# Kernel optimization log

Hardware: AMD Instinct MI355X
Metric: run time of the kernel (lower is better)

Reference implementation:

```python
import jax, jax.numpy as jnp
import numpy as np

EMBEDDING_DIM = 64
NUM_EMBEDDINGS = 512
COMMITMENT_COST = 0.25
DECAY = 0.99
EPSILON = 1e-5


def setup_inputs() -> dict:
    key = jax.random.key(0)
    k1, k2 = jax.random.split(key)
    inputs = jax.random.normal(k1, (64, 32, 32, EMBEDDING_DIM), dtype=jnp.float32)
    # VarianceScaling(uniform) init over [D, K]: scale ~ sqrt(3/fan_in)
    limit = np.sqrt(3.0 / EMBEDDING_DIM)
    embeddings = jax.random.uniform(
        k2, (EMBEDDING_DIM, NUM_EMBEDDINGS), dtype=jnp.float32,
        minval=-limit, maxval=limit)
    return {
        "inputs": inputs,
        "embeddings": embeddings,
        "ema_cluster_size_hidden": jnp.zeros((NUM_EMBEDDINGS,), jnp.float32),
        "ema_dw_hidden": jnp.zeros((EMBEDDING_DIM, NUM_EMBEDDINGS), jnp.float32),
        "counter": 0,  # EMA step counter before this call
    }


def reference(inputs, embeddings, ema_cluster_size_hidden, ema_dw_hidden, counter):
    # is_training=True path of VectorQuantizerEMA.__call__
    flat = inputs.reshape(-1, EMBEDDING_DIM)                        # [N, D]
    # squared L2 distances to each codebook vector: [N, K]
    distances = (jnp.sum(jnp.square(flat), 1, keepdims=True)
                 - 2.0 * jnp.matmul(flat, embeddings)
                 + jnp.sum(jnp.square(embeddings), 0, keepdims=True))
    encoding_indices_flat = jnp.argmax(-distances, 1)               # [N]
    encodings = jax.nn.one_hot(encoding_indices_flat, NUM_EMBEDDINGS,
                               dtype=distances.dtype)               # [N, K]
    encoding_indices = encoding_indices_flat.reshape(inputs.shape[:-1])
    quantized = embeddings.T[encoding_indices]                      # gather rows of [K, D]

    e_latent_loss = jnp.mean(jnp.square(jax.lax.stop_gradient(quantized) - inputs))
    loss = COMMITMENT_COST * e_latent_loss

    # --- EMA updates (haiku ExponentialMovingAverage with zero-debias) ---
    new_counter = counter + 1
    debias = 1.0 - DECAY ** new_counter
    cluster_size = jnp.sum(encodings, axis=0)                        # [K]
    hid_cs = ema_cluster_size_hidden * DECAY + cluster_size * (1.0 - DECAY)
    updated_ema_cluster_size = hid_cs / debias
    dw = jnp.matmul(flat.T, encodings)                               # [D, K]
    hid_dw = ema_dw_hidden * DECAY + dw * (1.0 - DECAY)
    updated_ema_dw = hid_dw / debias

    n = jnp.sum(updated_ema_cluster_size)
    stable_cs = ((updated_ema_cluster_size + EPSILON)
                 / (n + NUM_EMBEDDINGS * EPSILON) * n)
    new_embeddings = updated_ema_dw / stable_cs[None, :]             # [D, K]

    # straight-through estimator
    quantized_st = inputs + jax.lax.stop_gradient(quantized - inputs)

    avg_probs = jnp.mean(encodings, 0)
    perplexity = jnp.exp(-jnp.sum(avg_probs * jnp.log(avg_probs + 1e-10)))

    return (quantized_st, loss, perplexity, encoding_indices,
            new_embeddings, hid_cs, hid_dw)
```

## Files before the change

### kernel.cpp

```cpp
#include <hip/hip_runtime.h>
#include <math.h>

#define D 64
#define K 512
#define NROWS 65536
#define DECAY 0.99f
#define ONE_MINUS_DECAY (1.0f - 0.99f)
#define COMMIT 0.25f

#define WS_DWT    0
#define WS_CNT    32768
#define WS_LPART  33280
#define WS_ZERO4  8192
#define WS_ESQ    35328
#define WS_ET     35840
#define WS_EF     68608
#define WS_IDX    101376
#define WS_HIST   166912
#define WS_PERM   35840

#define OUT_Q     0
#define OUT_LOSS  4194304
#define OUT_PERP  4194305
#define OUT_IDX   4194306
#define OUT_NEMB  4259842
#define OUT_HCS   4292610
#define OUT_HDW   4293122

typedef _Float16 f16x8 __attribute__((ext_vector_type(8)));
typedef float    f32x16 __attribute__((ext_vector_type(16)));

__global__ void vq_prep(const float* __restrict__ emb,
                        float* __restrict__ ws)
{
    int i = blockIdx.x * 256 + threadIdx.x;
    if (i < WS_ZERO4) {
        ((float4*)ws)[i] = make_float4(0.f, 0.f, 0.f, 0.f);
    }
    if (i < K * D) {
        int k = i >> 6, d = i & 63;
        ws[WS_ET + i] = emb[d * K + k];
    }
    if (i < K) {
        float s = 0.f;
        for (int d = 0; d < D; ++d) { float v = emb[d * K + i]; s += v * v; }
        ws[WS_ESQ + i] = s;
    }
    if (i < 8192) {
        int l = i & 63, h = (i >> 6) & 1, s = (i >> 7) & 3, t = i >> 9;
        int col = t * 32 + (l & 31);
        int d0  = s * 16 + ((l >> 5) << 3);
        f16x8 frag;
#pragma unroll
        for (int j = 0; j < 8; ++j) {
            float v = emb[(d0 + j) * K + col];
            _Float16 hv = (_Float16)v;
            frag[j] = h ? (_Float16)(v - (float)hv) : hv;
        }
        ((f16x8*)(ws + WS_EF))[i] = frag;
    }
}

__global__ __launch_bounds__(256, 4)
void vq_main(const float* __restrict__ x,
             const float* __restrict__ e_sq,
             const float* __restrict__ e_t,
             const float* __restrict__ ef,
             float* __restrict__ out_q,
             float* __restrict__ out_idx,
             int*   __restrict__ idxN,
             float* __restrict__ lparts)
{
    __shared__ float sc_s[4][32];
    __shared__ int   id_s[4][32];
    __shared__ int   idx_f[32];

    const int tid  = threadIdx.x;
    const int w    = tid >> 6;
    const int l    = tid & 63;
    const int lr   = l & 31;
    const int hb   = l >> 5;
    const int row0 = blockIdx.x * 32;

    f16x8 ah[4], al[4];
    float xsq = 0.f;
    {
        const float* xr = x + (size_t)(row0 + lr) * D + hb * 8;
#pragma unroll
        for (int s = 0; s < 4; ++s) {
            float4 f0 = *(const float4*)(xr + s * 16);
            float4 f1 = *(const float4*)(xr + s * 16 + 4);
            float f[8] = {f0.x, f0.y, f0.z, f0.w, f1.x, f1.y, f1.z, f1.w};
#pragma unroll
            for (int j = 0; j < 8; ++j) {
                xsq = fmaf(f[j], f[j], xsq);
                _Float16 hv = (_Float16)f[j];
                ah[s][j] = hv;
                al[s][j] = (_Float16)(f[j] - (float)hv);
            }
        }
    }

    float    best[16];
    unsigned pack = 0u;
#pragma unroll
    for (int r = 0; r < 16; ++r) best[r] = 3.0e38f;

    const f16x8* __restrict__ efv = (const f16x8*)ef;

#pragma unroll 2
    for (int tt = 0; tt < 4; ++tt) {
        const int t = w * 4 + tt;
        f32x16 acc = {};
#pragma unroll
        for (int s = 0; s < 4; ++s) {
            f16x8 bh = efv[(t * 8 + s * 2 + 0) * 64 + l];
            f16x8 bl = efv[(t * 8 + s * 2 + 1) * 64 + l];
            acc = __builtin_amdgcn_mfma_f32_32x32x16_f16(al[s], bh, acc, 0, 0, 0);
            acc = __builtin_amdgcn_mfma_f32_32x32x16_f16(ah[s], bl, acc, 0, 0, 0);
            acc = __builtin_amdgcn_mfma_f32_32x32x16_f16(ah[s], bh, acc, 0, 0, 0);
        }

        const float eq = e_sq[t * 32 + lr];
#pragma unroll
        for (int r = 0; r < 16; ++r) {
            float sc = fmaf(-2.0f, acc[r], eq);
            bool better = sc < best[r];
            unsigned nb = (pack & ~(3u << (2 * r)))
                        | ((unsigned)tt << (2 * r));
            best[r] = better ? sc : best[r];
            pack    = better ? nb : pack;
        }
    }

#pragma unroll
    for (int r = 0; r < 16; ++r) {
        float b  = best[r];
        int   bk = (w * 4 + (int)((pack >> (2 * r)) & 3u)) * 32 + lr;
#pragma unroll
        for (int m = 16; m >= 1; m >>= 1) {
            float ob  = __shfl_xor(b, m, 64);
            int   obk = __shfl_xor(bk, m, 64);
            if (ob < b || (ob == b && obk < bk)) { b = ob; bk = obk; }
        }
        if (lr == 0) {
            int row = (r & 3) + 8 * (r >> 2) + 4 * hb;
            sc_s[w][row] = b;
            id_s[w][row] = bk;
        }
    }

    float xs_total = 0.f;
    if (w == 0) {
        float xs = xsq;
#pragma unroll
        for (int m = 32; m >= 1; m >>= 1) xs += __shfl_xor(xs, m, 64);
        xs_total = xs;
    }
    __syncthreads();

    if (tid < 32) {
        float b = sc_s[0][tid]; int bk = id_s[0][tid];
#pragma unroll
        for (int w2 = 1; w2 < 4; ++w2) {
            float ob = sc_s[w2][tid];
            int  obk = id_s[w2][tid];
            if (ob < b) { b = ob; bk = obk; }
        }
        idx_f[tid] = bk;
        out_idx[row0 + tid] = (float)bk;
        idxN[row0 + tid]    = bk;

        float lb = b;
#pragma unroll
        for (int m = 16; m >= 1; m >>= 1) lb += __shfl_xor(lb, m, 64);
        if (tid == 0)
            lparts[blockIdx.x] = lb + xs_total;
    }
    __syncthreads();

#pragma unroll
    for (int rr = 0; rr < 8; ++rr) {
        const int row = w * 8 + rr;
        const int kk  = idx_f[row];
        out_q[(size_t)(row0 + row) * D + l] = e_t[kk * D + l];
    }
}

__global__ __launch_bounds__(256)
void vq_hist(const int* __restrict__ idxN,
             int* __restrict__ hist)
{
    __shared__ int h[K];
    const int t = threadIdx.x;
    h[t] = 0; h[t + 256] = 0;
    __syncthreads();
    const int base = blockIdx.x * 1024;
#pragma unroll
    for (int it = 0; it < 4; ++it)
        atomicAdd(&h[idxN[base + it * 256 + t]], 1);
    __syncthreads();
    hist[blockIdx.x * K + t]       = h[t];
    hist[blockIdx.x * K + t + 256] = h[t + 256];
}

__global__ __launch_bounds__(512)
void vq_scatter(const int* __restrict__ hist,
                const int* __restrict__ idxN,
                int* __restrict__ cnt,
                int* __restrict__ perm)
{
    __shared__ int s[K];

    const int t = threadIdx.x;
    const int b = blockIdx.x;

    int run = 0, mybase = 0;
    for (int b2 = 0; b2 < 64; ++b2) {
        int h = hist[b2 * K + t];
        if (b2 == b) mybase = run;
        run += h;
    }
    if (b == 0) cnt[t] = run;

    s[t] = run;
    __syncthreads();
#pragma unroll
    for (int off = 1; off < K; off <<= 1) {
        int v = (t >= off) ? s[t - off] : 0;
        __syncthreads();
        s[t] += v;
        __syncthreads();
    }
    const int offs = s[t] - run;
    __syncthreads();
    s[t] = offs + mybase;
    __syncthreads();

#pragma unroll
    for (int it = 0; it < 2; ++it) {
        int row = b * 1024 + it * 512 + t;
        int kk  = idxN[row];
        int pos = atomicAdd(&s[kk], 1);
        perm[pos] = (row << 9) | kk;
    }
}

__global__ __launch_bounds__(256, 2)
void vq_dwsum(const int* __restrict__ perm,
              const float* __restrict__ x,
              float* __restrict__ dw_t)
{
    const int w = (blockIdx.x * 256 + threadIdx.x) >> 6;
    const int l = threadIdx.x & 63;

    int pv = 0;
    if (l < 32) pv = perm[w * 32 + l];

    float sum = 0.f;
    int kcur = -1;
#pragma unroll
    for (int e = 0; e < 32; ++e) {
        int pe  = __shfl(pv, e, 64);
        int kk  = pe & (K - 1);
        int row = pe >> 9;
        float xv = x[(size_t)row * D + l];
        if (kk != kcur) {
            if (kcur >= 0) atomicAdd(&dw_t[kcur * D + l], sum);
            kcur = kk; sum = xv;
        } else {
            sum += xv;
        }
    }
    atomicAdd(&dw_t[kcur * D + l], sum);
}

__global__ __launch_bounds__(256)
void vq_final(const int*   __restrict__ cnt,
              const float* __restrict__ lparts,
              const float* __restrict__ ema_csh,
              const int*   __restrict__ counter,
              const float* __restrict__ ema_dwh,
              const float* __restrict__ dw_t,
              float* __restrict__ out_loss,
              float* __restrict__ out_perp,
              float* __restrict__ out_hcs,
              float* __restrict__ out_nemb,
              float* __restrict__ out_hdw)
{
    __shared__ float s_red[4], s_red2[4];
    __shared__ float s_n;

    const int tid = threadIdx.x;
    const int b   = blockIdx.x;

    const int   cntr   = counter[0] + 1;
    const float debias = 1.0f - powf(DECAY, (float)cntr);

    const float c0 = (float)cnt[tid];
    const float c1 = (float)cnt[tid + 256];
    const float hid0 = ema_csh[tid] * DECAY + c0 * ONE_MINUS_DECAY;
    const float hid1 = ema_csh[tid + 256] * DECAY + c1 * ONE_MINUS_DECAY;
    const float upd0 = hid0 / debias;
    const float upd1 = hid1 / debias;

    float v = upd0 + upd1;
#pragma unroll
    for (int m = 32; m >= 1; m >>= 1) v += __shfl_xor(v, m, 64);
    if ((tid & 63) == 0) s_red[tid >> 6] = v;
    __syncthreads();
    if (tid == 0) s_n = s_red[0] + s_red[1] + s_red[2] + s_red[3];
    __syncthreads();
    const float n = s_n;

    const int i  = b * 256 + tid;
    const int kk = i & (K - 1);
    const int d  = i >> 9;
    const float updk   = (b & 1) ? upd1 : upd0;
    const float stable = (updk + 1e-5f) / (n + (float)K * 1e-5f) * n;
    const float hdw = ema_dwh[i] * DECAY + dw_t[kk * D + d] * ONE_MINUS_DECAY;
    out_hdw[i]  = hdw;
    out_nemb[i] = (hdw / debias) / stable;

    if (b == 0) {
        out_hcs[tid]       = hid0;
        out_hcs[tid + 256] = hid1;

        const float inv = 1.0f / (float)NROWS;
        float p0 = c0 * inv, p1 = c1 * inv;
        float ve = p0 * logf(p0 + 1e-10f) + p1 * logf(p1 + 1e-10f);
        float lp = 0.f;
#pragma unroll
        for (int j = 0; j < 8; ++j) lp += lparts[tid + 256 * j];
#pragma unroll
        for (int m = 32; m >= 1; m >>= 1) {
            ve += __shfl_xor(ve, m, 64);
            lp += __shfl_xor(lp, m, 64);
        }
        __syncthreads();
        if ((tid & 63) == 0) { s_red[tid >> 6] = ve; s_red2[tid >> 6] = lp; }
        __syncthreads();
        if (tid == 0) {
            float e = s_red[0] + s_red[1] + s_red[2] + s_red[3];
            float L = s_red2[0] + s_red2[1] + s_red2[2] + s_red2[3];
            out_loss[0] = COMMIT * L / (float)((size_t)NROWS * D);
            out_perp[0] = expf(-e);
        }
    }
}

extern "C" void kernel_launch(void* const* d_in, const int* in_sizes, int n_in,
                              void* d_out, int out_size, void* d_ws, size_t ws_size,
                              hipStream_t stream)
{
    const float* x_in    = (const float*)d_in[0];
    const float* emb     = (const float*)d_in[1];
    const float* ema_csh = (const float*)d_in[2];
    const float* ema_dwh = (const float*)d_in[3];
    const int*   counter = (const int*)d_in[4];

    float* ws  = (float*)d_ws;
    float* out = (float*)d_out;

    vq_prep<<<128, 256, 0, stream>>>(emb, ws);

    vq_main<<<NROWS / 32, 256, 0, stream>>>(
        x_in, ws + WS_ESQ, ws + WS_ET, ws + WS_EF,
        out + OUT_Q, out + OUT_IDX,
        (int*)(ws + WS_IDX), ws + WS_LPART);

    vq_hist<<<64, 256, 0, stream>>>(
        (const int*)(ws + WS_IDX), (int*)(ws + WS_HIST));

    vq_scatter<<<64, 512, 0, stream>>>(
        (const int*)(ws + WS_HIST), (const int*)(ws + WS_IDX),
        (int*)(ws + WS_CNT), (int*)(ws + WS_PERM));

    vq_dwsum<<<512, 256, 0, stream>>>(
        (const int*)(ws + WS_PERM), x_in, ws + WS_DWT);

    vq_final<<<128, 256, 0, stream>>>(
        (const int*)(ws + WS_CNT), ws + WS_LPART, ema_csh, counter,
        ema_dwh, ws + WS_DWT,
        out + OUT_LOSS, out + OUT_PERP, out + OUT_HCS,
        out + OUT_NEMB, out + OUT_HDW);
}
```

Measured before the change: 139.5 us.

## Give each wave its own rows over all codes and drop cross-wave reduction

In vq_main, each wavefront now owns 32 rows and scans all 512 codebook entries, instead of four waves splitting the codes for the same 32 rows. This removes the shared-memory argmin merge and both block barriers, and the grid shrinks to 512 blocks of 128 rows. The argmin shuffle packs an order-preserving float key together with the index into one 64-bit value, so each step needs one shuffle and one compare. vq_dwsum now handles 64 permuted entries per wave to cut the number of atomics, in exchange for longer serial loops per wave and more codebook fragment loads per wave.

After: 143.0 us. 1.03x slower.

```diff
diff --git a/kernel.cpp b/kernel.cpp
--- a/kernel.cpp
+++ b/kernel.cpp
@@ -71,16 +71,14 @@
              int*   __restrict__ idxN,
              float* __restrict__ lparts)
 {
-    __shared__ float sc_s[4][32];
-    __shared__ int   id_s[4][32];
-    __shared__ int   idx_f[32];
+    __shared__ int idx_s[4][32];
 
     const int tid  = threadIdx.x;
     const int w    = tid >> 6;
     const int l    = tid & 63;
     const int lr   = l & 31;
     const int hb   = l >> 5;
-    const int row0 = blockIdx.x * 32;
+    const int row0 = blockIdx.x * 128 + w * 32;
 
     f16x8 ah[4], al[4];
     float xsq = 0.f;
@@ -102,88 +100,84 @@
     }
 
     float    best[16];
-    unsigned pack = 0u;
+    unsigned packlo = 0u, packhi = 0u;
 #pragma unroll
     for (int r = 0; r < 16; ++r) best[r] = 3.0e38f;
 
     const f16x8* __restrict__ efv = (const f16x8*)ef;
 
 #pragma unroll 2
-    for (int tt = 0; tt < 4; ++tt) {
-        const int t = w * 4 + tt;
+    for (int tt = 0; tt < 16; ++tt) {
         f32x16 acc = {};
 #pragma unroll
         for (int s = 0; s < 4; ++s) {
-            f16x8 bh = efv[(t * 8 + s * 2 + 0) * 64 + l];
-            f16x8 bl = efv[(t * 8 + s * 2 + 1) * 64 + l];
+            f16x8 bh = efv[(tt * 8 + s * 2 + 0) * 64 + l];
+            f16x8 bl = efv[(tt * 8 + s * 2 + 1) * 64 + l];
             acc = __builtin_amdgcn_mfma_f32_32x32x16_f16(al[s], bh, acc, 0, 0, 0);
             acc = __builtin_amdgcn_mfma_f32_32x32x16_f16(ah[s], bl, acc, 0, 0, 0);
             acc = __builtin_amdgcn_mfma_f32_32x32x16_f16(ah[s], bh, acc, 0, 0, 0);
         }
 
-        const float eq = e_sq[t * 32 + lr];
+        const float eq = e_sq[tt * 32 + lr];
 #pragma unroll
         for (int r = 0; r < 16; ++r) {
             float sc = fmaf(-2.0f, acc[r], eq);
             bool better = sc < best[r];
-            unsigned nb = (pack & ~(3u << (2 * r)))
-                        | ((unsigned)tt << (2 * r));
             best[r] = better ? sc : best[r];
-            pack    = better ? nb : pack;
-        }
-    }
-
+            if (r < 8) {
+                unsigned nb = (packlo & ~(15u << (4 * r)))
+                            | ((unsigned)tt << (4 * r));
+                packlo = better ? nb : packlo;
+            } else {
+                unsigned nb = (packhi & ~(15u << (4 * (r - 8))))
+                            | ((unsigned)tt << (4 * (r - 8)));
+                packhi = better ? nb : packhi;
+            }
+        }
+    }
+
+    float sum_best = 0.f;
 #pragma unroll
     for (int r = 0; r < 16; ++r) {
-        float b  = best[r];
-        int   bk = (w * 4 + (int)((pack >> (2 * r)) & 3u)) * 32 + lr;
+        unsigned tt4 = ((r < 8) ? (packlo >> (4 * r))
+                                : (packhi >> (4 * (r - 8)))) & 15u;
+        int bk = ((int)tt4 << 5) | lr;
+        unsigned sb = __float_as_uint(best[r]);
+        sb ^= (unsigned)((int)sb >> 31) | 0x80000000u;
+        unsigned long long key =
+            ((unsigned long long)sb << 32) | (unsigned)bk;
 #pragma unroll
         for (int m = 16; m >= 1; m >>= 1) {
-            float ob  = __shfl_xor(b, m, 64);
-            int   obk = __shfl_xor(bk, m, 64);
-            if (ob < b || (ob == b && obk < bk)) { b = ob; bk = obk; }
-        }
+            unsigned long long o = __shfl_xor(key, m, 64);
+            key = (o < key) ? o : key;
+        }
+        unsigned wb = (unsigned)(key >> 32);
+        wb ^= ~(unsigned)((int)wb >> 31) | 0x80000000u;
+        sum_best += __uint_as_float(wb);
         if (lr == 0) {
-            int row = (r & 3) + 8 * (r >> 2) + 4 * hb;
-            sc_s[w][row] = b;
-            id_s[w][row] = bk;
-        }
-    }
-
-    float xs_total = 0.f;
-    if (w == 0) {
+            int ro = (r & 3) + 8 * (r >> 2) + 4 * hb;
+            idx_s[w][ro] = (int)(key & 511u);
+        }
+    }
+
+    {
         float xs = xsq;
 #pragma unroll
         for (int m = 32; m >= 1; m >>= 1) xs += __shfl_xor(xs, m, 64);
-        xs_total = xs;
-    }
-    __syncthreads();
-
-    if (tid < 32) {
-        float b = sc_s[0][tid]; int bk = id_s[0][tid];
-#pragma unroll
-        for (int w2 = 1; w2 < 4; ++w2) {
-            float ob = sc_s[w2][tid];
-            int  obk = id_s[w2][tid];
-            if (ob < b) { b = ob; bk = obk; }
-        }
-        idx_f[tid] = bk;
-        out_idx[row0 + tid] = (float)bk;
-        idxN[row0 + tid]    = bk;
-
-        float lb = b;
-#pragma unroll
-        for (int m = 16; m >= 1; m >>= 1) lb += __shfl_xor(lb, m, 64);
-        if (tid == 0)
-            lparts[blockIdx.x] = lb + xs_total;
-    }
-    __syncthreads();
-
-#pragma unroll
-    for (int rr = 0; rr < 8; ++rr) {
-        const int row = w * 8 + rr;
-        const int kk  = idx_f[row];
-        out_q[(size_t)(row0 + row) * D + l] = e_t[kk * D + l];
+        float tb = sum_best + __shfl_xor(sum_best, 32, 64);
+        if (l == 0)
+            lparts[blockIdx.x * 4 + w] = xs + tb;
+    }
+
+    if (l < 32) {
+        int bk = idx_s[w][l];
+        out_idx[row0 + l] = (float)bk;
+        idxN[row0 + l]    = bk;
+    }
+#pragma unroll
+    for (int rr = 0; rr < 32; ++rr) {
+        const int kk = idx_s[w][rr];
+        out_q[(size_t)(row0 + rr) * D + l] = e_t[kk * D + l];
     }
 }
 
@@ -254,13 +248,11 @@
     const int w = (blockIdx.x * 256 + threadIdx.x) >> 6;
     const int l = threadIdx.x & 63;
 
-    int pv = 0;
-    if (l < 32) pv = perm[w * 32 + l];
+    const int pv = perm[w * 64 + l];
 
     float sum = 0.f;
     int kcur = -1;
-#pragma unroll
-    for (int e = 0; e < 32; ++e) {
+    for (int e = 0; e < 64; ++e) {
         int pe  = __shfl(pv, e, 64);
         int kk  = pe & (K - 1);
         int row = pe >> 9;
@@ -364,7 +356,7 @@
 
     vq_prep<<<128, 256, 0, stream>>>(emb, ws);
 
-    vq_main<<<NROWS / 32, 256, 0, stream>>>(
+    vq_main<<<NROWS / 128, 256, 0, stream>>>(
         x_in, ws + WS_ESQ, ws + WS_ET, ws + WS_EF,
         out + OUT_Q, out + OUT_IDX,
         (int*)(ws + WS_IDX), ws + WS_LPART);
@@ -376,7 +368,7 @@
         (const int*)(ws + WS_HIST), (const int*)(ws + WS_IDX),
         (int*)(ws + WS_CNT), (int*)(ws + WS_PERM));
 
-    vq_dwsum<<<512, 256, 0, stream>>>(
+    vq_dwsum<<<256, 256, 0, stream>>>(
         (const int*)(ws + WS_PERM), x_in, ws + WS_DWT);
 
     vq_final<<<128, 256, 0, stream>>>(
```
